# Kernel tuning notes

Measured on AMD Instinct MI355X. Metric: run time of the kernel, lower is better.

The kernel has to match this reference:

```python
import jax, jax.numpy as jnp
import numpy as np

KERNEL_SIZE = 5
SIGMA_SPATIAL = 1.0
SIGMA_RANGE = 0.1
EPS = 1e-8


def _spatial_kernel(k: int, sigma: float) -> jnp.ndarray:
    coords = jnp.arange(k, dtype=jnp.float32) - (k - 1) / 2.0
    d2 = coords[:, None] ** 2 + coords[None, :] ** 2
    return jnp.exp(-d2 / (2.0 * sigma ** 2))


def setup_inputs() -> dict:
    key = jax.random.key(0)
    x = jax.random.uniform(key, (4, 3, 512, 512), dtype=jnp.float32)
    spatial_kernel = _spatial_kernel(KERNEL_SIZE, SIGMA_SPATIAL)
    return {"x": x, "spatial_kernel": spatial_kernel}


def reference(x, spatial_kernel):
    # x: (B, C, H, W); spatial_kernel: (k, k)
    k = KERNEL_SIZE
    p = k // 2
    B, C, H, W = x.shape
    xp = jnp.pad(x, ((0, 0), (0, 0), (p, p), (p, p)), mode="reflect")
    # Stack the k*k shifted windows -> (B, C, H, W, k*k). This is the
    # vectorized equivalent of the per-pixel patch extraction.
    patches = jnp.stack(
        [xp[:, :, di:di + H, dj:dj + W] for di in range(k) for dj in range(k)],
        axis=-1,
    )
    center = x[..., None]  # (B, C, H, W, 1)
    range_w = jnp.exp(-((patches - center) ** 2) / (2.0 * SIGMA_RANGE ** 2))
    weights = range_w * spatial_kernel.reshape(-1)  # broadcast over last axis
    weights_norm = weights / (jnp.sum(weights, axis=-1, keepdims=True) + EPS)
    return jnp.sum(patches * weights_norm, axis=-1)  # (B, C, H, W)
```

## Files before the change

kernel.cpp:

```cpp
#include <hip/hip_runtime.h>

#define IMG_H 512
#define IMG_W 512

#define LOG2E 1.4426950408889634f
#define HALF_LOG2E 0.7213475204444817f

#define EXP2_SCALE 8388608.0f
#define EXP2_BIAS 1065055989.0f

typedef float v2f __attribute__((ext_vector_type(2)));

static __device__ __forceinline__ v2f pk_fma(v2f a, v2f b, v2f c) {
  v2f d;
  asm("v_pk_fma_f32 %0, %1, %2, %3" : "=v"(d) : "v"(a), "v"(b), "v"(c));
  return d;
}
static __device__ __forceinline__ v2f pk_nfma(v2f a, v2f b, v2f c) {
  v2f d;
  asm("v_pk_fma_f32 %0, %1, %2, %3 neg_lo:[1,0,0] neg_hi:[1,0,0]"
      : "=v"(d) : "v"(a), "v"(b), "v"(c));
  return d;
}
static __device__ __forceinline__ v2f pk_add(v2f a, v2f b) {
  v2f d;
  asm("v_pk_add_f32 %0, %1, %2" : "=v"(d) : "v"(a), "v"(b));
  return d;
}
static __device__ __forceinline__ float fast_rcp(float x) {
  return __builtin_amdgcn_rcpf(x);
}

__global__ __launch_bounds__(256) void bilateral_kernel(
    const float* __restrict__ x, float* __restrict__ out) {
  const int t   = blockIdx.x * 64 + threadIdx.x;
  const int rp  = blockIdx.y * 4 + threadIdx.y;
  const int hy0 = rp * 2;
  const int plane = blockIdx.z;

  const size_t pbase = (size_t)plane * (IMG_H * IMG_W);
  const float* __restrict__ img = x + pbase;

  int rows[6];
#pragma unroll
  for (int k = 0; k < 6; ++k) {
    int r = hy0 + k - 2;
    r = (r < 0) ? -r : ((r >= IMG_H) ? (2 * IMG_H - 2 - r) : r);
    rows[k] = r;
  }

  v2f w2[6][3];
  v2f wS[6][2];

  const bool edgeBlock = (blockIdx.x == 0) | (blockIdx.x == gridDim.x - 1);
  if (!edgeBlock) {
#pragma unroll
    for (int k = 0; k < 6; ++k) {
      const float2* __restrict__ r2 = (const float2*)(img + (size_t)rows[k] * IMG_W);
      float2 L = r2[t - 1], C = r2[t], R = r2[t + 1];
      w2[k][0] = (v2f){L.x, L.y};
      w2[k][1] = (v2f){C.x, C.y};
      w2[k][2] = (v2f){R.x, R.y};
      wS[k][0] = (v2f){L.y, C.x};
      wS[k][1] = (v2f){C.y, R.x};
    }
  } else {
    const int li = (t > 0) ? t - 1 : 0;
    const int ri = (t < IMG_W / 2 - 1) ? t + 1 : IMG_W / 2 - 1;
    const bool le = (t == 0);
    const bool re = (t == IMG_W / 2 - 1);
#pragma unroll
    for (int k = 0; k < 6; ++k) {
      const float2* __restrict__ r2 = (const float2*)(img + (size_t)rows[k] * IMG_W);
      float2 L = r2[li], C = r2[t], R = r2[ri];
      float wm2 = le ? R.x : L.x;
      float wm1 = le ? C.y : L.y;
      float wp2 = re ? C.x : R.x;
      float wp3 = re ? L.y : R.y;
      w2[k][0] = (v2f){wm2, wm1};
      w2[k][1] = (v2f){C.x, C.y};
      w2[k][2] = (v2f){wp2, wp3};
      wS[k][0] = (v2f){wm1, C.x};
      wS[k][1] = (v2f){C.y, wp2};
    }
  }

  const float Ap = sqrtf(50.0f * LOG2E * EXP2_SCALE);
  const v2f A2 = {Ap, Ap};

  v2f ws[2] = {{0.f, 0.f}, {0.f, 0.f}};
  v2f vs[2] = {{0.f, 0.f}, {0.f, 0.f}};
  v2f nca[2];
#pragma unroll
  for (int p = 0; p < 2; ++p) {
    nca[p].x = -w2[p + 2][1].x * Ap;
    nca[p].y = -w2[p + 2][1].y * Ap;
  }

#pragma unroll
  for (int k = 0; k < 6; ++k) {
    v2f vals[5] = {w2[k][0], wS[k][0], w2[k][1], wS[k][1], w2[k][2]};
#pragma unroll
    for (int p = 0; p < 2; ++p) {
      const int di = k - p;
      if (di < 0 || di > 4) continue;
#pragma unroll
      for (int dj = 0; dj < 5; ++dj) {
        const int d2s = (di - 2) * (di - 2) + (dj - 2) * (dj - 2);
        const float bias = EXP2_BIAS - HALF_LOG2E * (float)d2s * EXP2_SCALE;
        v2f val = vals[dj];
        v2f da = pk_fma(val, A2, nca[p]);
        v2f tt = pk_nfma(da, da, (v2f){bias, bias});
        v2f rw;
        rw.x = __uint_as_float((unsigned)tt.x);
        rw.y = __uint_as_float((unsigned)tt.y);
        ws[p] = pk_add(ws[p], rw);
        vs[p] = pk_fma(rw, val, vs[p]);
      }
    }
  }

#pragma unroll
  for (int p = 0; p < 2; ++p) {
    float2 res;
    res.x = vs[p].x * fast_rcp(ws[p].x);
    res.y = vs[p].y * fast_rcp(ws[p].y);
    float2* __restrict__ op =
        (float2*)(out + pbase + (size_t)(hy0 + p) * IMG_W);
    op[t] = res;
  }
}

extern "C" void kernel_launch(void* const* d_in, const int* in_sizes, int n_in,
                              void* d_out, int out_size, void* d_ws, size_t ws_size,
                              hipStream_t stream) {
  const float* x = (const float*)d_in[0];
  float* out = (float*)d_out;

  const int planes = in_sizes[0] / (IMG_H * IMG_W);

  dim3 block(64, 4, 1);
  dim3 grid(IMG_W / 128, IMG_H / 8, planes);
  bilateral_kernel<<<grid, block, 0, stream>>>(x, out);
}
```

Baseline: 18.02 us.

## Process four columns per thread with float4 loads and staged row loading

Each thread now computes a 2x4 output patch instead of 2x2, loading float4 per row and building seven overlapping pairs so neighbouring columns share loaded values. The grid halves in x, and the edge/interior split is replaced by a single clamped path. Rows are loaded and consumed in stages to limit live registers. This halves the thread count and raises per-thread register use, so occupancy may drop while load instructions per output fall.

New measurement: 17.02 us. 5.6% less time.

```diff
diff --git a/kernel.cpp b/kernel.cpp
--- a/kernel.cpp
+++ b/kernel.cpp
@@ -31,11 +31,58 @@
   return __builtin_amdgcn_rcpf(x);
 }
 
+struct RowPairs {
+  v2f p[7];
+};
+
+static __device__ __forceinline__ RowPairs build_pairs(const float* __restrict__ rowp,
+                                                       int t, int li, int ri,
+                                                       bool le, bool re) {
+  const float4* __restrict__ r4 = (const float4*)rowp;
+  float4 L = r4[li];
+  float4 C = r4[t];
+  float4 R = r4[ri];
+  float m2 = le ? C.z : L.z;
+  float m1 = le ? C.y : L.w;
+  float q4 = re ? C.z : R.x;
+  float q5 = re ? C.y : R.y;
+  RowPairs r;
+  r.p[0] = (v2f){m2, m1};
+  r.p[1] = (v2f){m1, C.x};
+  r.p[2] = (v2f){C.x, C.y};
+  r.p[3] = (v2f){C.y, C.z};
+  r.p[4] = (v2f){C.z, C.w};
+  r.p[5] = (v2f){C.w, q4};
+  r.p[6] = (v2f){q4, q5};
+  return r;
+}
+
+template <int DI>
+static __device__ __forceinline__ void accum_row(const RowPairs& r, v2f A2,
+                                                 const v2f nca[2], v2f ws[2],
+                                                 v2f vs[2]) {
+#pragma unroll
+  for (int dj = 0; dj < 5; ++dj) {
+    const int d2s = (DI - 2) * (DI - 2) + (dj - 2) * (dj - 2);
+    const float bias = EXP2_BIAS - HALF_LOG2E * (float)d2s * EXP2_SCALE;
+#pragma unroll
+    for (int q = 0; q < 2; ++q) {
+      v2f val = r.p[dj + 2 * q];
+      v2f da = pk_fma(val, A2, nca[q]);
+      v2f tt = pk_nfma(da, da, (v2f){bias, bias});
+      v2f rw;
+      rw.x = __uint_as_float((unsigned)tt.x);
+      rw.y = __uint_as_float((unsigned)tt.y);
+      ws[q] = pk_add(ws[q], rw);
+      vs[q] = pk_fma(rw, val, vs[q]);
+    }
+  }
+}
+
 __global__ __launch_bounds__(256) void bilateral_kernel(
     const float* __restrict__ x, float* __restrict__ out) {
   const int t   = blockIdx.x * 64 + threadIdx.x;
-  const int rp  = blockIdx.y * 4 + threadIdx.y;
-  const int hy0 = rp * 2;
+  const int hy0 = (blockIdx.y * 4 + threadIdx.y) * 2;
   const int plane = blockIdx.z;
 
   const size_t pbase = (size_t)plane * (IMG_H * IMG_W);
@@ -45,88 +92,63 @@
 #pragma unroll
   for (int k = 0; k < 6; ++k) {
     int r = hy0 + k - 2;
-    r = (r < 0) ? -r : ((r >= IMG_H) ? (2 * IMG_H - 2 - r) : r);
-    rows[k] = r;
+    rows[k] = (r < 0) ? -r : ((r >= IMG_H) ? (2 * IMG_H - 2 - r) : r);
   }
 
-  v2f w2[6][3];
-  v2f wS[6][2];
-
-  const bool edgeBlock = (blockIdx.x == 0) | (blockIdx.x == gridDim.x - 1);
-  if (!edgeBlock) {
-#pragma unroll
-    for (int k = 0; k < 6; ++k) {
-      const float2* __restrict__ r2 = (const float2*)(img + (size_t)rows[k] * IMG_W);
-      float2 L = r2[t - 1], C = r2[t], R = r2[t + 1];
-      w2[k][0] = (v2f){L.x, L.y};
-      w2[k][1] = (v2f){C.x, C.y};
-      w2[k][2] = (v2f){R.x, R.y};
-      wS[k][0] = (v2f){L.y, C.x};
-      wS[k][1] = (v2f){C.y, R.x};
-    }
-  } else {
-    const int li = (t > 0) ? t - 1 : 0;
-    const int ri = (t < IMG_W / 2 - 1) ? t + 1 : IMG_W / 2 - 1;
-    const bool le = (t == 0);
-    const bool re = (t == IMG_W / 2 - 1);
-#pragma unroll
-    for (int k = 0; k < 6; ++k) {
-      const float2* __restrict__ r2 = (const float2*)(img + (size_t)rows[k] * IMG_W);
-      float2 L = r2[li], C = r2[t], R = r2[ri];
-      float wm2 = le ? R.x : L.x;
-      float wm1 = le ? C.y : L.y;
-      float wp2 = re ? C.x : R.x;
-      float wp3 = re ? L.y : R.y;
-      w2[k][0] = (v2f){wm2, wm1};
-      w2[k][1] = (v2f){C.x, C.y};
-      w2[k][2] = (v2f){wp2, wp3};
-      wS[k][0] = (v2f){wm1, C.x};
-      wS[k][1] = (v2f){C.y, wp2};
-    }
-  }
+  const int li = (t > 0) ? t - 1 : 0;
+  const int ri = (t < IMG_W / 4 - 1) ? t + 1 : IMG_W / 4 - 1;
+  const bool le = (t == 0);
+  const bool re = (t == IMG_W / 4 - 1);
 
   const float Ap = sqrtf(50.0f * LOG2E * EXP2_SCALE);
   const v2f A2 = {Ap, Ap};
 
-  v2f ws[2] = {{0.f, 0.f}, {0.f, 0.f}};
-  v2f vs[2] = {{0.f, 0.f}, {0.f, 0.f}};
-  v2f nca[2];
+  v2f ws[2][2] = {{{0.f, 0.f}, {0.f, 0.f}}, {{0.f, 0.f}, {0.f, 0.f}}};
+  v2f vs[2][2] = {{{0.f, 0.f}, {0.f, 0.f}}, {{0.f, 0.f}, {0.f, 0.f}}};
+
+  RowPairs r2 = build_pairs(img + (size_t)rows[2] * IMG_W, t, li, ri, le, re);
+  RowPairs r3 = build_pairs(img + (size_t)rows[3] * IMG_W, t, li, ri, le, re);
+
+  v2f nca[2][2];
 #pragma unroll
-  for (int p = 0; p < 2; ++p) {
-    nca[p].x = -w2[p + 2][1].x * Ap;
-    nca[p].y = -w2[p + 2][1].y * Ap;
+  for (int q = 0; q < 2; ++q) {
+    nca[0][q] = pk_nfma(r2.p[2 + 2 * q], A2, (v2f){0.f, 0.f});
+    nca[1][q] = pk_nfma(r3.p[2 + 2 * q], A2, (v2f){0.f, 0.f});
   }
 
-#pragma unroll
-  for (int k = 0; k < 6; ++k) {
-    v2f vals[5] = {w2[k][0], wS[k][0], w2[k][1], wS[k][1], w2[k][2]};
-#pragma unroll
-    for (int p = 0; p < 2; ++p) {
-      const int di = k - p;
-      if (di < 0 || di > 4) continue;
-#pragma unroll
-      for (int dj = 0; dj < 5; ++dj) {
-        const int d2s = (di - 2) * (di - 2) + (dj - 2) * (dj - 2);
-        const float bias = EXP2_BIAS - HALF_LOG2E * (float)d2s * EXP2_SCALE;
-        v2f val = vals[dj];
-        v2f da = pk_fma(val, A2, nca[p]);
-        v2f tt = pk_nfma(da, da, (v2f){bias, bias});
-        v2f rw;
-        rw.x = __uint_as_float((unsigned)tt.x);
-        rw.y = __uint_as_float((unsigned)tt.y);
-        ws[p] = pk_add(ws[p], rw);
-        vs[p] = pk_fma(rw, val, vs[p]);
-      }
-    }
+  accum_row<2>(r2, A2, nca[0], ws[0], vs[0]);
+  accum_row<1>(r2, A2, nca[1], ws[1], vs[1]);
+  accum_row<3>(r3, A2, nca[0], ws[0], vs[0]);
+  accum_row<2>(r3, A2, nca[1], ws[1], vs[1]);
+
+  {
+    RowPairs r = build_pairs(img + (size_t)rows[0] * IMG_W, t, li, ri, le, re);
+    accum_row<0>(r, A2, nca[0], ws[0], vs[0]);
+  }
+  {
+    RowPairs r = build_pairs(img + (size_t)rows[1] * IMG_W, t, li, ri, le, re);
+    accum_row<1>(r, A2, nca[0], ws[0], vs[0]);
+    accum_row<0>(r, A2, nca[1], ws[1], vs[1]);
+  }
+  {
+    RowPairs r = build_pairs(img + (size_t)rows[4] * IMG_W, t, li, ri, le, re);
+    accum_row<4>(r, A2, nca[0], ws[0], vs[0]);
+    accum_row<3>(r, A2, nca[1], ws[1], vs[1]);
+  }
+  {
+    RowPairs r = build_pairs(img + (size_t)rows[5] * IMG_W, t, li, ri, le, re);
+    accum_row<4>(r, A2, nca[1], ws[1], vs[1]);
   }
 
 #pragma unroll
   for (int p = 0; p < 2; ++p) {
-    float2 res;
-    res.x = vs[p].x * fast_rcp(ws[p].x);
-    res.y = vs[p].y * fast_rcp(ws[p].y);
-    float2* __restrict__ op =
-        (float2*)(out + pbase + (size_t)(hy0 + p) * IMG_W);
+    float4 res;
+    res.x = vs[p][0].x * fast_rcp(ws[p][0].x);
+    res.y = vs[p][0].y * fast_rcp(ws[p][0].y);
+    res.z = vs[p][1].x * fast_rcp(ws[p][1].x);
+    res.w = vs[p][1].y * fast_rcp(ws[p][1].y);
+    float4* __restrict__ op =
+        (float4*)(out + pbase + (size_t)(hy0 + p) * IMG_W);
     op[t] = res;
   }
 }
@@ -140,6 +162,6 @@
   const int planes = in_sizes[0] / (IMG_H * IMG_W);
 
   dim3 block(64, 4, 1);
-  dim3 grid(IMG_W / 128, IMG_H / 8, planes);
+  dim3 grid(IMG_W / 256, IMG_H / 8, planes);
   bilateral_kernel<<<grid, block, 0, stream>>>(x, out);
 }
```
